# Kernel tuning notes

Measured on AMD Instinct MI355X. Metric: run time of the kernel, lower is better.

The kernel has to match this reference:

```python
import jax, jax.numpy as jnp
import numpy as np

P, L, H = 3, 4, 6          # window size, num scales, num heads
EPS = 1e-5                 # LayerNorm eps (PyTorch default)


def setup_inputs() -> dict:
    key = jax.random.key(0)
    B, T, D = 8, 4096, 768
    ks = jax.random.split(key, 12)
    s = 0.02
    w = lambda k, shape: (jax.random.normal(k, shape, jnp.float32) * s)
    z = lambda n: jnp.zeros((n,), jnp.float32)
    return {
        "x": jax.random.normal(ks[0], (B, T, D), jnp.float32),
        "ln_g": jnp.ones((D,), jnp.float32),
        "ln_b": z(D),
        "qw": w(ks[1], (D, D)), "qb": z(D),
        "kw": w(ks[2], (D, D)), "kb": z(D),
        "vw": w(ks[3], (D, D)), "vb": z(D),
        "inw": w(ks[4], (3 * D, D)), "inb": z(3 * D),   # MHA in_proj
        "mow": w(ks[5], (D, D)), "mob": z(D),            # MHA out_proj
        "ow": w(ks[6], (D, D)), "ob": z(D),              # output_proj
    }


def _layernorm(x, g, b):
    mu = jnp.mean(x, -1, keepdims=True)
    var = jnp.mean((x - mu) ** 2, -1, keepdims=True)
    return (x - mu) * jax.lax.rsqrt(var + EPS) * g + b


def _mha_windows(q, k, v, inw, inb, mow, mob):
    # q,k,v: [B, W, P, D] -- batched tiny attention over all windows at once
    B, W, Pw, D = q.shape
    hd = D // H
    wq, wk, wv = inw[:D], inw[D:2 * D], inw[2 * D:]
    bq, bk, bv = inb[:D], inb[D:2 * D], inb[2 * D:]
    qp = (q @ wq.T + bq).reshape(B, W, Pw, H, hd)
    kp = (k @ wk.T + bk).reshape(B, W, Pw, H, hd)
    vp = (v @ wv.T + bv).reshape(B, W, Pw, H, hd)
    scores = jnp.einsum('bwqhd,bwkhd->bwhqk', qp, kp) / jnp.sqrt(jnp.float32(hd))
    attn = jax.nn.softmax(scores, axis=-1)
    o = jnp.einsum('bwhqk,bwkhd->bwqhd', attn, vp).reshape(B, W, Pw, D)
    return o @ mow.T + mob


def reference(x, ln_g, ln_b, qw, qb, kw, kb, vw, vb, inw, inb, mow, mob, ow, ob):
    B, T, D = x.shape
    xn = _layernorm(x, ln_g, ln_b)
    Q = xn @ qw.T + qb
    K = xn @ kw.T + kb
    V = xn @ vw.T + vb
    acc = jnp.zeros_like(x)
    for kk in range(L):
        scale = P ** kk
        if T < scale:
            continue
        Lp = T // scale
        pool = lambda z: z[:, :Lp * scale].reshape(B, Lp, scale, D).mean(axis=2)
        pQ, pK, pV = pool(Q), pool(K), pool(V)
        W = Lp // P
        if W == 0:
            continue
        win = lambda z: z[:, :W * P].reshape(B, W, P, D)
        o = _mha_windows(win(pQ), win(pK), win(pV), inw, inb, mow, mob)
        so = o.reshape(B, W * P, D)                       # concat of windows
        idx = (jnp.arange(T) * (W * P)) // T              # nearest interp to T
        up = so[:, idx]
        acc = acc + jax.nn.gelu(up, approximate=False)    # exact GELU (torch default)
    out = acc @ ow.T + ob
    return x + out
```

## Files before the change

### kernel.cpp

```cpp
#include <hip/hip_runtime.h>
#include <stdint.h>

typedef short s16x8 __attribute__((ext_vector_type(8)));
typedef float f32x4 __attribute__((ext_vector_type(4)));

__device__ __forceinline__ unsigned short f2bf(float f) {
  unsigned u = __builtin_bit_cast(unsigned, f);
  u = (u + 0x7FFFu + ((u >> 16) & 1u)) >> 16;
  return (unsigned short)u;
}
__device__ __forceinline__ float bf2f(unsigned short h) {
  unsigned u = ((unsigned)h) << 16;
  return __builtin_bit_cast(float, u);
}

__device__ __forceinline__ void gload_lds16(const void* g, void* l) {
  __builtin_amdgcn_global_load_lds((__attribute__((address_space(1))) void*)g,
                                   (__attribute__((address_space(3))) void*)l,
                                   16, 0, 0);
}

__global__ __launch_bounds__(256)
void mstr_prep(const float* __restrict__ qw, const float* __restrict__ kw,
               const float* __restrict__ vw, const float* __restrict__ inw,
               const float* __restrict__ mow, const float* __restrict__ ow,
               const float* __restrict__ inb, const float* __restrict__ qb,
               const float* __restrict__ kb, const float* __restrict__ vb,
               unsigned short* __restrict__ inwB, unsigned short* __restrict__ wT,
               unsigned short* __restrict__ mowB, unsigned short* __restrict__ owB,
               float* __restrict__ bc, float* __restrict__ zb)
{
  const long n1 = 589824;
  __shared__ float tile[32][33];
  int b = blockIdx.x, tid = threadIdx.x;
  if (b < 11520) {
    long i = (long)b * 256 + tid;
    if (i < 3 * n1)      inwB[i] = f2bf(inw[i]);
    else if (i < 4 * n1) mowB[i - 3 * n1] = f2bf(mow[i - 3 * n1]);
    else                 owB[i - 4 * n1] = f2bf(ow[i - 4 * n1]);
  } else if (b < 13248) {
    int z = b - 11520;
    int s = z % 3, r = z / 3;
    int jb = r % 24, kb = r / 24;
    const float* src = (s == 0) ? qw : (s == 1) ? kw : vw;
    unsigned short* dst = wT + (long)s * n1;
    int tx = tid & 31, ty = tid >> 5;
    int j0 = jb * 32, k0 = kb * 32;
#pragma unroll
    for (int i = 0; i < 4; ++i)
      tile[ty + i * 8][tx] = src[(long)(j0 + ty + i * 8) * 768 + k0 + tx];
    __syncthreads();
#pragma unroll
    for (int i = 0; i < 4; ++i)
      dst[(long)(k0 + ty + i * 8) * 768 + j0 + tx] = f2bf(tile[tx][ty + i * 8]);
  } else {
    int gid = (b - 13248) * 256 + tid;
    if (gid < 768) zb[gid] = 0.f;
    int s = gid / 768, c = gid - s * 768;
    const float* bb = (s == 0) ? qb : (s == 1) ? kb : vb;
    const float* wrow = inw + (long)(s * 768 + c) * 768;
    float a = inb[s * 768 + c];
    for (int j = 0; j < 768; ++j) a += bb[j] * wrow[j];
    bc[gid] = a;
  }
}

__global__ __launch_bounds__(256)
void mstr_ln(const float* __restrict__ x, const float* __restrict__ g,
             const float* __restrict__ bt, unsigned short* __restrict__ xn)
{
  int blk = blockIdx.x;
  int bb = blk / 4095, t = blk - bb * 4095;
  const float* xr = x + ((long)bb * 4096 + t) * 768;
  unsigned short* orow = xn + (long)blk * 768;
  int tid = threadIdx.x;
  float v0 = xr[tid], v1 = xr[tid + 256], v2 = xr[tid + 512];
  float s = v0 + v1 + v2;
  float s2 = v0 * v0 + v1 * v1 + v2 * v2;
#pragma unroll
  for (int o = 32; o > 0; o >>= 1) { s += __shfl_down(s, o, 64); s2 += __shfl_down(s2, o, 64); }
  __shared__ float rs[4], rq[4];
  int lane = tid & 63, wid = tid >> 6;
  if (lane == 0) { rs[wid] = s; rq[wid] = s2; }
  __syncthreads();
  float S = rs[0] + rs[1] + rs[2] + rs[3];
  float S2 = rq[0] + rq[1] + rq[2] + rq[3];
  float mu = S * (1.0f / 768.0f);
  float var = S2 * (1.0f / 768.0f) - mu * mu;
  float rstd = rsqrtf(var + 1e-5f);
  __builtin_nontemporal_store(f2bf((v0 - mu) * rstd * g[tid] + bt[tid]), &orow[tid]);
  __builtin_nontemporal_store(f2bf((v1 - mu) * rstd * g[tid + 256] + bt[tid + 256]), &orow[tid + 256]);
  __builtin_nontemporal_store(f2bf((v2 - mu) * rstd * g[tid + 512] + bt[tid + 512]), &orow[tid + 512]);
}

template<int EPI>
__global__ __launch_bounds__(256, 4)
void mstr_gemm(const unsigned short* __restrict__ A, int M,
               const unsigned short* __restrict__ W,
               const float* __restrict__ bias,
               unsigned short* out0, unsigned short* out1, unsigned short* out2,
               float* outf, const float* xadd,
               int rowDiv, int rowStride, int NC, int nwg, long zoff)
{
  __shared__ char smem[49152];
  if (zoff) {
    long zo = (long)blockIdx.y * zoff;
    A += zo; W += zo; out0 += zo; out1 += zo; out2 += zo;
  }
  int orig = blockIdx.x;
  int swq = nwg >> 3, swr = nwg & 7;
  int xcd = orig & 7, sidx = orig >> 3;
  int wg = (xcd < swr ? xcd * (swq + 1) : swr * (swq + 1) + (xcd - swr) * swq) + sidx;
  int rowp = wg / NC, colp = wg - rowp * NC;

  const int tid = threadIdx.x;
  const int lane = tid & 63;
  const int wid = tid >> 6;
  const int wr = wid >> 1, wc = wid & 1;
  const long row0 = (long)rowp * 128;
  const int col0 = colp * 128;

  const int sr = tid >> 2;
  const int sc = (((tid & 3) ^ ((tid >> 3) & 3)) << 3);
  long a0r = row0 + sr;       if (a0r >= M) a0r = M - 1;
  long a1r = row0 + sr + 64;  if (a1r >= M) a1r = M - 1;
  const unsigned short* Ag0 = A + a0r * 768 + sc;
  const unsigned short* Ag1 = A + a1r * 768 + sc;
  const unsigned short* Bg0 = W + (long)(col0 + sr) * 768 + sc;
  const unsigned short* Bg1 = W + (long)(col0 + sr + 64) * 768 + sc;
  char* ldsT = smem + tid * 16;

  const int fr = lane & 15;
  const int g4 = lane >> 4;
  const int cx = ((g4 ^ ((fr >> 1) & 3)) << 4);
  const int aoff = (wr * 64 + fr) * 64 + cx;
  const int boff = 8192 + (wc * 64 + fr) * 64 + cx;

  f32x4 acc[4][4] = {};

#define MSTAGE(T, BO) { int kk_ = (T) * 32; \
    gload_lds16(Ag0 + kk_, ldsT + (BO)); \
    gload_lds16(Ag1 + kk_, ldsT + (BO) + 4096); \
    gload_lds16(Bg0 + kk_, ldsT + (BO) + 8192); \
    gload_lds16(Bg1 + kk_, ldsT + (BO) + 12288); }

  MSTAGE(0, 0)
  int stBo = 16384;
  int rdBo = 0;
  for (int t = 0; t < 24; ++t) {
    if (t < 23) {
      MSTAGE(t + 1, stBo)
      stBo += 16384; if (stBo == 49152) stBo = 0;
      asm volatile("s_waitcnt vmcnt(4)" ::: "memory");
    } else {
      asm volatile("s_waitcnt vmcnt(0)" ::: "memory");
    }
    __builtin_amdgcn_s_barrier();
    const int bo = rdBo;
    rdBo += 16384; if (rdBo == 49152) rdBo = 0;
    s16x8 af[4], bfv[4];
#pragma unroll
    for (int m = 0; m < 4; ++m) af[m] = *(const s16x8*)(smem + bo + aoff + m * 1024);
#pragma unroll
    for (int n = 0; n < 4; ++n) bfv[n] = *(const s16x8*)(smem + bo + boff + n * 1024);
    __builtin_amdgcn_s_setprio(1);
#pragma unroll
    for (int m = 0; m < 4; ++m)
#pragma unroll
      for (int n = 0; n < 4; ++n)
        acc[m][n] = __builtin_amdgcn_mfma_f32_16x16x32_bf16(af[m], bfv[n], acc[m][n], 0, 0, 0);
    __builtin_amdgcn_s_setprio(0);
  }
#undef MSTAGE

  int seg = (col0 >= 1536) ? 2 : (col0 >= 768 ? 1 : 0);
  unsigned short* outp = (seg == 0) ? out0 : (seg == 1) ? out1 : out2;
  int csub = seg * 768;
#pragma unroll
  for (int m = 0; m < 4; ++m) {
#pragma unroll
    for (int r = 0; r < 4; ++r) {
      long gr = row0 + wr * 64 + m * 16 + g4 * 4 + r;
      if (gr < M) {
        long orow;
        if (EPI == 1) {
          orow = gr;
        } else {
          int qq = (int)gr / rowDiv;
          orow = (long)qq * rowStride + ((int)gr - qq * rowDiv);
        }
#pragma unroll
        for (int n = 0; n < 4; ++n) {
          int c = col0 + wc * 64 + n * 16 + fr;
          float v = acc[m][n][r] + bias[c];
          if (EPI == 1) {
            long o = gr * 768 + c;
            __builtin_nontemporal_store(v + xadd[o], &outf[o]);
          } else if (EPI == 2) {
            v = 0.5f * v * (1.0f + erff(v * 0.70710678118654752f));
            __builtin_nontemporal_store(f2bf(v), &outp[orow * 768 + (c - csub)]);
          } else {
            __builtin_nontemporal_store(f2bf(v), &outp[orow * 768 + (c - csub)]);
          }
        }
      }
    }
  }
}

__global__ __launch_bounds__(384)
void mstr_pool(unsigned short* qp, unsigned short* kp, unsigned short* vp,
               int srcOff, int dstOff, int Ndst)
{
  unsigned short* p = (blockIdx.y == 0) ? qp : (blockIdx.y == 1) ? kp : vp;
  int tok = blockIdx.x;
  int bb = tok / Ndst, j = tok - bb * Ndst;
  long sb = ((long)bb * 6063 + srcOff + 3 * j) * 768 + threadIdx.x * 2;
  long db = ((long)bb * 6063 + dstOff + j) * 768 + threadIdx.x * 2;
  unsigned a = *(const unsigned*)(p + sb);
  unsigned b = *(const unsigned*)(p + sb + 768);
  unsigned c = *(const unsigned*)(p + sb + 1536);
  float lo = (bf2f((unsigned short)a) + bf2f((unsigned short)b) + bf2f((unsigned short)c)) * (1.0f / 3.0f);
  float hi = (bf2f((unsigned short)(a >> 16)) + bf2f((unsigned short)(b >> 16)) + bf2f((unsigned short)(c >> 16))) * (1.0f / 3.0f);
  unsigned o = (unsigned)f2bf(lo) | ((unsigned)f2bf(hi) << 16);
  *(unsigned*)(p + db) = o;
}

__global__ __launch_bounds__(256)
void mstr_attn(unsigned short* qp, unsigned short* kp, unsigned short* vp, int nwaves)
{
  int gw = blockIdx.x * 4 + (threadIdx.x >> 6);
  if (gw >= nwaves) return;
  int lane = threadIdx.x & 63;
  int win = gw / 6, h = gw - win * 6;
  int bb = win / 2021, ww = win - bb * 2021;
  int row0;
  if (ww < 1365)      row0 = 3 * ww;
  else if (ww < 1820) row0 = 4095 + 3 * (ww - 1365);
  else if (ww < 1971) row0 = 5460 + 3 * (ww - 1820);
  else                row0 = 5913 + 3 * (ww - 1971);
  long base = ((long)bb * 6063 + row0) * 768 + h * 128 + lane * 2;
  float q[3][2], k[3][2], v[3][2];
#pragma unroll
  for (int i = 0; i < 3; ++i) {
    unsigned uq = *(const unsigned*)(qp + base + i * 768);
    unsigned uk = *(const unsigned*)(kp + base + i * 768);
    unsigned uv = *(const unsigned*)(vp + base + i * 768);
    q[i][0] = bf2f((unsigned short)uq); q[i][1] = bf2f((unsigned short)(uq >> 16));
    k[i][0] = bf2f((unsigned short)uk); k[i][1] = bf2f((unsigned short)(uk >> 16));
    v[i][0] = bf2f((unsigned short)uv); v[i][1] = bf2f((unsigned short)(uv >> 16));
  }
  float s[3][3];
#pragma unroll
  for (int i = 0; i < 3; ++i)
#pragma unroll
    for (int j = 0; j < 3; ++j)
      s[i][j] = q[i][0] * k[j][0] + q[i][1] * k[j][1];
#pragma unroll
  for (int st = 1; st < 64; st <<= 1) {
#pragma unroll
    for (int i = 0; i < 3; ++i)
#pragma unroll
      for (int j = 0; j < 3; ++j)
        s[i][j] += __shfl_xor(s[i][j], st, 64);
  }
  const float scl = 0.088388347648318447f;
#pragma unroll
  for (int i = 0; i < 3; ++i) {
    float s0 = s[i][0] * scl, s1 = s[i][1] * scl, s2 = s[i][2] * scl;
    float m = fmaxf(s0, fmaxf(s1, s2));
    float e0 = __expf(s0 - m), e1 = __expf(s1 - m), e2 = __expf(s2 - m);
    float inv = 1.0f / (e0 + e1 + e2);
    e0 *= inv; e1 *= inv; e2 *= inv;
    float o0 = e0 * v[0][0] + e1 * v[1][0] + e2 * v[2][0];
    float o1 = e0 * v[0][1] + e1 * v[1][1] + e2 * v[2][1];
    unsigned o = (unsigned)f2bf(o0) | ((unsigned)f2bf(o1) << 16);
    *(unsigned*)(qp + base + i * 768) = o;
  }
}

__global__ __launch_bounds__(256)
void mstr_gelusum(const unsigned short* __restrict__ omo, unsigned short* __restrict__ acc)
{
  long gid = (long)blockIdx.x * 256 + threadIdx.x;
  int d2 = (int)(gid % 384);
  long row = gid / 384;
  int bb = (int)(row >> 12);
  int t = (int)(row & 4095);
  const int NkA[4] = {4095, 1365, 453, 150};
  const int soA[4] = {0, 4095, 5460, 5913};
  float a0 = 0.f, a1 = 0.f;
#pragma unroll
  for (int kk = 0; kk < 4; ++kk) {
    int idx = (t * NkA[kk]) >> 12;
    long tok = (long)bb * 6063 + soA[kk] + idx;
    unsigned u = *(const unsigned*)(omo + tok * 768 + d2 * 2);
    a0 += bf2f((unsigned short)u);
    a1 += bf2f((unsigned short)(u >> 16));
  }
  unsigned o = (unsigned)f2bf(a0) | ((unsigned)f2bf(a1) << 16);
  *(unsigned*)(acc + row * 768 + d2 * 2) = o;
}

extern "C" void kernel_launch(void* const* d_in, const int* in_sizes, int n_in,
                              void* d_out, int out_size, void* d_ws, size_t ws_size,
                              hipStream_t stream)
{
  const float* x   = (const float*)d_in[0];
  const float* lng = (const float*)d_in[1];
  const float* lnb = (const float*)d_in[2];
  const float* qw  = (const float*)d_in[3];
  const float* qb  = (const float*)d_in[4];
  const float* kw  = (const float*)d_in[5];
  const float* kb  = (const float*)d_in[6];
  const float* vw  = (const float*)d_in[7];
  const float* vb  = (const float*)d_in[8];
  const float* inw = (const float*)d_in[9];
  const float* inb = (const float*)d_in[10];
  const float* mob = (const float*)d_in[12];
  const float* ow  = (const float*)d_in[13];
  const float* ob  = (const float*)d_in[14];

  const long n1 = 589824;
  char* ws = (char*)d_ws;
  size_t off = 0;
  auto alloc = [&](size_t bytes) -> char* {
    char* p = ws + off;
    off += (bytes + 255) & ~(size_t)255;
    return p;
  };
  unsigned short* Wc = (unsigned short*)alloc((size_t)5 * n1 * 2);
  float* bc = (float*)alloc(2304 * 4);
  float* zb = (float*)alloc(768 * 4);
  size_t fixed = off;

  int g = 0;
  const int cands[4] = {8, 4, 2, 1};
  for (int ci = 0; ci < 4; ++ci) {
    int c = cands[ci];
    size_t need = fixed + (size_t)c * 4096 * 768 * 2
                + 2 * (size_t)c * 6063 * 768 * 2
                + 1024;
    if (need <= ws_size) { g = c; break; }
  }
  if (!g) return;

  char* GR = ws + fixed;
  unsigned short* xnacc = (unsigned short*)GR;
  unsigned short* qp = xnacc + (size_t)g * 4096 * 768;
  unsigned short* kp = qp + (size_t)g * 6063 * 768;
  unsigned short* inwB = (unsigned short*)GR;
  unsigned short* wT   = inwB + 3 * n1;

  unsigned short* mowB = Wc + 3 * n1;
  unsigned short* owB  = Wc + 4 * n1;

  mstr_prep<<<dim3(13257), dim3(256), 0, stream>>>(qw, kw, vw, inw, (const float*)d_in[11], ow,
                                                   inb, qb, kb, vb, inwB, wT, mowB, owB, bc, zb);
  mstr_gemm<0><<<dim3(36, 3), dim3(256), 0, stream>>>(inwB, 768, wT, zb, Wc, Wc, Wc,
                                                      nullptr, nullptr, 768, 768, 6, 36, n1);

  int ng = 8 / g;
  for (int gi = 0; gi < ng; ++gi) {
    const float* xg = x + (long)gi * g * 4096 * 768;
    unsigned short* vp = (unsigned short*)d_out + (long)gi * g * 4096 * 768 * 2;
    mstr_ln<<<dim3(g * 4095), dim3(256), 0, stream>>>(xg, lng, lnb, xnacc);
    int M1 = g * 4095, gb1 = (M1 + 127) / 128;
    int nwg1 = gb1 * 18;
    mstr_gemm<0><<<dim3(nwg1), dim3(256), 0, stream>>>(xnacc, M1, Wc, bc,
                                                       qp, kp, vp, nullptr, nullptr,
                                                       4095, 6063, 18, nwg1, 0);
    mstr_pool<<<dim3(g * 1365, 3), dim3(384), 0, stream>>>(qp, kp, vp, 0, 4095, 1365);
    mstr_pool<<<dim3(g * 453, 3), dim3(384), 0, stream>>>(qp, kp, vp, 4095, 5460, 453);
    mstr_pool<<<dim3(g * 150, 3), dim3(384), 0, stream>>>(qp, kp, vp, 5460, 5913, 150);
    int nw = g * 2021 * 6;
    mstr_attn<<<dim3((nw + 3) / 4), dim3(256), 0, stream>>>(qp, kp, vp, nw);
    int M2 = g * 6063;
    int nwg2 = ((M2 + 127) / 128) * 6;
    mstr_gemm<2><<<dim3(nwg2), dim3(256), 0, stream>>>(qp, M2, mowB, mob, kp, kp, kp,
                                                       nullptr, nullptr, M2, 0, 6, nwg2, 0);
    mstr_gelusum<<<dim3(g * 6144), dim3(256), 0, stream>>>(kp, xnacc);
    int M3 = g * 4096;
    int nwg3 = (M3 / 128) * 6;
    mstr_gemm<1><<<dim3(nwg3), dim3(256), 0, stream>>>(xnacc, M3, owB, ob, nullptr, nullptr, nullptr,
                                                       (float*)d_out + (long)gi * g * 4096 * 768, xg,
                                                       M3, 0, 6, nwg3, 0);
  }
}
```

Measured before the change: 624.4 us.

## Load GEMM B fragments directly into registers, keep only A in LDS

```diff
diff --git a/kernel.cpp b/kernel.cpp
--- a/kernel.cpp
+++ b/kernel.cpp
@@ -102,7 +102,7 @@
                float* outf, const float* xadd,
                int rowDiv, int rowStride, int NC, int nwg, long zoff)
 {
-  __shared__ char smem[49152];
+  __shared__ char smem[32768];
   if (zoff) {
     long zo = (long)blockIdx.y * zoff;
     A += zo; W += zo; out0 += zo; out1 += zo; out2 += zo;
@@ -126,51 +126,55 @@
   long a1r = row0 + sr + 64;  if (a1r >= M) a1r = M - 1;
   const unsigned short* Ag0 = A + a0r * 768 + sc;
   const unsigned short* Ag1 = A + a1r * 768 + sc;
-  const unsigned short* Bg0 = W + (long)(col0 + sr) * 768 + sc;
-  const unsigned short* Bg1 = W + (long)(col0 + sr + 64) * 768 + sc;
   char* ldsT = smem + tid * 16;
 
   const int fr = lane & 15;
   const int g4 = lane >> 4;
   const int cx = ((g4 ^ ((fr >> 1) & 3)) << 4);
   const int aoff = (wr * 64 + fr) * 64 + cx;
-  const int boff = 8192 + (wc * 64 + fr) * 64 + cx;
+
+  const unsigned short* Bp = W + (long)(col0 + wc * 64 + fr) * 768 + g4 * 8;
 
   f32x4 acc[4][4] = {};
+  s16x8 bA[4], bB[4];
 
 #define MSTAGE(T, BO) { int kk_ = (T) * 32; \
     gload_lds16(Ag0 + kk_, ldsT + (BO)); \
-    gload_lds16(Ag1 + kk_, ldsT + (BO) + 4096); \
-    gload_lds16(Bg0 + kk_, ldsT + (BO) + 8192); \
-    gload_lds16(Bg1 + kk_, ldsT + (BO) + 12288); }
-
+    gload_lds16(Ag1 + kk_, ldsT + (BO) + 4096); }
+
+#pragma unroll
+  for (int n = 0; n < 4; ++n) bA[n] = *(const s16x8*)(Bp + n * 12288);
   MSTAGE(0, 0)
-  int stBo = 16384;
-  int rdBo = 0;
-  for (int t = 0; t < 24; ++t) {
-    if (t < 23) {
-      MSTAGE(t + 1, stBo)
-      stBo += 16384; if (stBo == 49152) stBo = 0;
-      asm volatile("s_waitcnt vmcnt(4)" ::: "memory");
-    } else {
-      asm volatile("s_waitcnt vmcnt(0)" ::: "memory");
-    }
-    __builtin_amdgcn_s_barrier();
-    const int bo = rdBo;
-    rdBo += 16384; if (rdBo == 49152) rdBo = 0;
-    s16x8 af[4], bfv[4];
-#pragma unroll
-    for (int m = 0; m < 4; ++m) af[m] = *(const s16x8*)(smem + bo + aoff + m * 1024);
-#pragma unroll
-    for (int n = 0; n < 4; ++n) bfv[n] = *(const s16x8*)(smem + bo + boff + n * 1024);
-    __builtin_amdgcn_s_setprio(1);
-#pragma unroll
-    for (int m = 0; m < 4; ++m)
-#pragma unroll
-      for (int n = 0; n < 4; ++n)
-        acc[m][n] = __builtin_amdgcn_mfma_f32_16x16x32_bf16(af[m], bfv[n], acc[m][n], 0, 0, 0);
-    __builtin_amdgcn_s_setprio(0);
-  }
+  MSTAGE(1, 8192)
+  asm volatile("s_waitcnt vmcnt(2)" ::: "memory");
+  __builtin_amdgcn_s_barrier();
+
+#define GBODY(T, BU, BL) { \
+    if ((T) + 1 < 24) { long ko_ = ((long)(T) + 1) * 32; \
+      _Pragma("unroll") \
+      for (int n = 0; n < 4; ++n) BL[n] = *(const s16x8*)(Bp + n * 12288 + ko_); } \
+    if ((T) + 2 < 24) MSTAGE((T) + 2, (((T) + 2) & 3) * 8192) \
+    if ((T) < 22)      asm volatile("s_waitcnt vmcnt(6)" ::: "memory"); \
+    else if ((T) == 22) asm volatile("s_waitcnt vmcnt(4)" ::: "memory"); \
+    else               asm volatile("s_waitcnt vmcnt(0)" ::: "memory"); \
+    __builtin_amdgcn_s_barrier(); \
+    const char* sb_ = smem + ((T) & 3) * 8192; \
+    s16x8 af[4]; \
+    _Pragma("unroll") \
+    for (int m = 0; m < 4; ++m) af[m] = *(const s16x8*)(sb_ + aoff + m * 1024); \
+    __builtin_amdgcn_s_setprio(1); \
+    _Pragma("unroll") \
+    for (int m = 0; m < 4; ++m) \
+      _Pragma("unroll") \
+      for (int n = 0; n < 4; ++n) \
+        acc[m][n] = __builtin_amdgcn_mfma_f32_16x16x32_bf16(af[m], BU[n], acc[m][n], 0, 0, 0); \
+    __builtin_amdgcn_s_setprio(0); }
+
+  for (int t = 0; t < 24; t += 2) {
+    GBODY(t, bA, bB)
+    GBODY(t + 1, bB, bA)
+  }
+#undef GBODY
 #undef MSTAGE
 
   int seg = (col0 >= 1536) ? 2 : (col0 >= 768 ? 1 : 0);
```

Result: slower. 841.3 us (+34.7%).
